# Performance work log

Hardware: AMD Instinct MI355X
Metric: run time of the kernel (lower is better)

Reference implementation:

```python
import jax, jax.numpy as jnp
import numpy as np

KNN_K = 3  # module hard-codes top-3 farthest sememes (torch.sort descending)


def setup_inputs() -> dict:
    key = jax.random.key(0)
    k1, k2, k3 = jax.random.split(key, 3)
    V, H = 50257, 1024
    L, W, S = 256, 16, 32
    embedding = jax.random.normal(k1, (V, H), dtype=jnp.float32)
    word_ids = jax.random.randint(k2, (L, W), 0, V, dtype=jnp.int32)
    sememe_ids = jax.random.randint(k3, (L, W, S), 0, V, dtype=jnp.int32)
    return {"embedding": embedding, "word_ids": word_ids, "sememe_ids": sememe_ids}


def reference(embedding, word_ids, sememe_ids):
    # embedding: [V,H]; word_ids: [L,W]; sememe_ids: [L,W,S]
    w = embedding[word_ids]                  # [L,W,H]  word embeddings (s)
    sm = embedding[sememe_ids]               # [L,W,S,H] sememe embeddings
    # F.pairwise_distance(s, sememe_tensor, p=2): L2 per sememe
    dist = jnp.linalg.norm(sm - w[:, :, None, :], axis=-1)  # [L,W,S]
    # torch.sort(distance, descending=True)[1][:3] -> 3 farthest sememes
    _, idx = jax.lax.top_k(dist, KNN_K)                      # [L,W,K]
    sel = jnp.take_along_axis(sm, idx[..., None], axis=2)    # [L,W,K,H]
    # cat([knn_mean.unsqueeze(0), s], 0).mean(0) == (knn_mean + s) / 2
    per_word = 0.5 * (sel.mean(axis=2) + w)                  # [L,W,H]
    # stack(span).mean(0): mean over words in each label
    return per_word.mean(axis=1)                             # [L,H]
```

## Files before the change

kernel.cpp:

```cpp
#include <hip/hip_runtime.h>


#define HDIM 1024
#define SNUM 32
#define WNUM 16
#define KNN  3

__global__ __launch_bounds__(256) void knn_dist_kernel(
    const float* __restrict__ emb,
    const int*   __restrict__ word_ids,
    const int*   __restrict__ sem_ids,
    float*       __restrict__ dist,
    int nj)
{
    const int wave = threadIdx.x >> 6;
    const int lane = threadIdx.x & 63;
    const int j    = blockIdx.x * 4 + wave;
    if (j >= nj) return;
    const int b    = j >> 5;

    const int wid = word_ids[b];
    const int sid = sem_ids[j];

    const float* wrow = emb + (size_t)wid * HDIM + 4 * lane;
    const float* srow = emb + (size_t)sid * HDIM + 4 * lane;

    const float4 w0 = *(const float4*)(wrow + 0);
    const float4 w1 = *(const float4*)(wrow + 256);
    const float4 w2 = *(const float4*)(wrow + 512);
    const float4 w3 = *(const float4*)(wrow + 768);
    const float4 s0 = *(const float4*)(srow + 0);
    const float4 s1 = *(const float4*)(srow + 256);
    const float4 s2 = *(const float4*)(srow + 512);
    const float4 s3 = *(const float4*)(srow + 768);

    float d = 0.0f;
    {
        float dx = s0.x - w0.x, dy = s0.y - w0.y, dz = s0.z - w0.z, dw = s0.w - w0.w;
        d += dx * dx + dy * dy + dz * dz + dw * dw;
    }
    {
        float dx = s1.x - w1.x, dy = s1.y - w1.y, dz = s1.z - w1.z, dw = s1.w - w1.w;
        d += dx * dx + dy * dy + dz * dz + dw * dw;
    }
    {
        float dx = s2.x - w2.x, dy = s2.y - w2.y, dz = s2.z - w2.z, dw = s2.w - w2.w;
        d += dx * dx + dy * dy + dz * dz + dw * dw;
    }
    {
        float dx = s3.x - w3.x, dy = s3.y - w3.y, dz = s3.z - w3.z, dw = s3.w - w3.w;
        d += dx * dx + dy * dy + dz * dz + dw * dw;
    }

    #pragma unroll
    for (int off = 32; off >= 1; off >>= 1)
        d += __shfl_xor(d, off, 64);

    if (lane == 0) dist[j] = d;
}

__global__ __launch_bounds__(256) void knn_select_kernel(
    const float* __restrict__ dist,
    const int*   __restrict__ word_ids,
    const int*   __restrict__ sem_ids,
    int*         __restrict__ sel,
    int nb)
{
    const int b = blockIdx.x * 256 + threadIdx.x;
    if (b >= nb) return;

    float dl[SNUM];
    #pragma unroll
    for (int s = 0; s < SNUM; ++s) dl[s] = dist[b * SNUM + s];

    unsigned chosen = 0;
    #pragma unroll
    for (int k = 0; k < KNN; ++k) {
        float best = -1.0f;
        int   bi   = 0;
        #pragma unroll
        for (int s = 0; s < SNUM; ++s) {
            if (!((chosen >> s) & 1u) && dl[s] > best) { best = dl[s]; bi = s; }
        }
        chosen |= (1u << bi);
        sel[b * 4 + k] = sem_ids[b * SNUM + bi];
    }
    sel[b * 4 + 3] = word_ids[b];
}

__global__ __launch_bounds__(256) void knn_out_kernel(
    const float* __restrict__ emb,
    const int*   __restrict__ sel,
    float*       __restrict__ out)
{
    const int l = blockIdx.x >> 2;
    const int q = blockIdx.x & 3;
    const int h = q * 256 + threadIdx.x;

    __shared__ int s_ids[WNUM * 4];
    if (threadIdx.x < WNUM * 4) s_ids[threadIdx.x] = sel[l * WNUM * 4 + threadIdx.x];
    __syncthreads();

    const float third = 1.0f / 3.0f;
    float acc = 0.0f;
    #pragma unroll
    for (int w = 0; w < WNUM; ++w) {
        const float e0 = emb[(size_t)s_ids[w * 4 + 0] * HDIM + h];
        const float e1 = emb[(size_t)s_ids[w * 4 + 1] * HDIM + h];
        const float e2 = emb[(size_t)s_ids[w * 4 + 2] * HDIM + h];
        const float ew = emb[(size_t)s_ids[w * 4 + 3] * HDIM + h];
        acc += (e0 + e1 + e2) * third + ew;
    }
    out[(size_t)l * HDIM + h] = acc * (0.5f / 16.0f);
}

extern "C" void kernel_launch(void* const* d_in, const int* in_sizes, int n_in,
                              void* d_out, int out_size, void* d_ws, size_t ws_size,
                              hipStream_t stream) {
    const float* emb  = (const float*)d_in[0];
    const int*   wids = (const int*)d_in[1];
    const int*   sids = (const int*)d_in[2];
    float*       out  = (float*)d_out;

    const int nb = in_sizes[1];
    const int nj = in_sizes[2];
    const int L  = out_size / HDIM;

    float* dist = (float*)d_ws;
    int*   sel  = (int*)((char*)d_ws + (size_t)nj * 4);

    knn_dist_kernel<<<dim3((nj + 3) / 4), dim3(256), 0, stream>>>(emb, wids, sids, dist, nj);
    knn_select_kernel<<<dim3((nb + 255) / 256), dim3(256), 0, stream>>>(dist, wids, sids, sel, nb);
    knn_out_kernel<<<dim3(L * 4), dim3(256), 0, stream>>>(emb, sel, out);
}
```

Baseline: 107.6 us.

## Split distance kernel by hidden-dim quarters with per-word block and partial sums

Each block now handles one word and one quarter of the hidden dimension, with each wave computing 8 sememes. The word row slice is loaded once per wave instead of once per sememe, and partial distances go to four workspace slices. The select kernel sums those four partials before doing top-3. This cuts redundant word-embedding reads and raises memory-level parallelism per wave, at the cost of a larger workspace, extra partial writes and more shuffle reductions.

```diff
diff --git a/kernel.cpp b/kernel.cpp
--- a/kernel.cpp
+++ b/kernel.cpp
@@ -10,68 +10,77 @@
     const float* __restrict__ emb,
     const int*   __restrict__ word_ids,
     const int*   __restrict__ sem_ids,
-    float*       __restrict__ dist,
+    float*       __restrict__ dist_part,
     int nj)
 {
     const int wave = threadIdx.x >> 6;
     const int lane = threadIdx.x & 63;
-    const int j    = blockIdx.x * 4 + wave;
-    if (j >= nj) return;
-    const int b    = j >> 5;
+    const int blk  = blockIdx.x;
+    const int b    = blk >> 2;
+    const int quarter = blk & 3;
 
-    const int wid = word_ids[b];
-    const int sid = sem_ids[j];
+    const int base_s = b * SNUM + wave * 8;
+    const int col    = quarter * 256 + 4 * lane;
 
-    const float* wrow = emb + (size_t)wid * HDIM + 4 * lane;
-    const float* srow = emb + (size_t)sid * HDIM + 4 * lane;
+    const int4 sa = *(const int4*)(sem_ids + base_s);
+    const int4 sb = *(const int4*)(sem_ids + base_s + 4);
+    const int  wid = word_ids[b];
 
-    const float4 w0 = *(const float4*)(wrow + 0);
-    const float4 w1 = *(const float4*)(wrow + 256);
-    const float4 w2 = *(const float4*)(wrow + 512);
-    const float4 w3 = *(const float4*)(wrow + 768);
-    const float4 s0 = *(const float4*)(srow + 0);
-    const float4 s1 = *(const float4*)(srow + 256);
-    const float4 s2 = *(const float4*)(srow + 512);
-    const float4 s3 = *(const float4*)(srow + 768);
+    const float4 w = *(const float4*)(emb + (size_t)wid * HDIM + col);
 
-    float d = 0.0f;
-    {
-        float dx = s0.x - w0.x, dy = s0.y - w0.y, dz = s0.z - w0.z, dw = s0.w - w0.w;
-        d += dx * dx + dy * dy + dz * dz + dw * dw;
-    }
-    {
-        float dx = s1.x - w1.x, dy = s1.y - w1.y, dz = s1.z - w1.z, dw = s1.w - w1.w;
-        d += dx * dx + dy * dy + dz * dz + dw * dw;
-    }
-    {
-        float dx = s2.x - w2.x, dy = s2.y - w2.y, dz = s2.z - w2.z, dw = s2.w - w2.w;
-        d += dx * dx + dy * dy + dz * dz + dw * dw;
-    }
-    {
-        float dx = s3.x - w3.x, dy = s3.y - w3.y, dz = s3.z - w3.z, dw = s3.w - w3.w;
-        d += dx * dx + dy * dy + dz * dz + dw * dw;
-    }
+    const int sids[8] = {sa.x, sa.y, sa.z, sa.w, sb.x, sb.y, sb.z, sb.w};
+    float4 sv[8];
+    #pragma unroll
+    for (int k = 0; k < 8; ++k)
+        sv[k] = *(const float4*)(emb + (size_t)sids[k] * HDIM + col);
 
     #pragma unroll
-    for (int off = 32; off >= 1; off >>= 1)
-        d += __shfl_xor(d, off, 64);
-
-    if (lane == 0) dist[j] = d;
+    for (int k = 0; k < 8; ++k) {
+        const float dx = sv[k].x - w.x;
+        const float dy = sv[k].y - w.y;
+        const float dz = sv[k].z - w.z;
+        const float dw = sv[k].w - w.w;
+        float d = (dx * dx + dy * dy) + (dz * dz + dw * dw);
+        #pragma unroll
+        for (int off = 32; off >= 1; off >>= 1)
+            d += __shfl_xor(d, off, 64);
+        if (lane == 0)
+            dist_part[(size_t)quarter * nj + base_s + k] = d;
+    }
 }
 
 __global__ __launch_bounds__(256) void knn_select_kernel(
-    const float* __restrict__ dist,
+    const float* __restrict__ dist_part,
     const int*   __restrict__ word_ids,
     const int*   __restrict__ sem_ids,
     int*         __restrict__ sel,
-    int nb)
+    int nb, int nj)
 {
     const int b = blockIdx.x * 256 + threadIdx.x;
     if (b >= nb) return;
 
+    float4 acc[8];
+    #pragma unroll
+    for (int i = 0; i < 8; ++i) acc[i] = make_float4(0.f, 0.f, 0.f, 0.f);
+
+    #pragma unroll
+    for (int q = 0; q < 4; ++q) {
+        const float4* p = (const float4*)(dist_part + (size_t)q * nj + b * SNUM);
+        #pragma unroll
+        for (int i = 0; i < 8; ++i) {
+            const float4 v = p[i];
+            acc[i].x += v.x; acc[i].y += v.y; acc[i].z += v.z; acc[i].w += v.w;
+        }
+    }
+
     float dl[SNUM];
     #pragma unroll
-    for (int s = 0; s < SNUM; ++s) dl[s] = dist[b * SNUM + s];
+    for (int i = 0; i < 8; ++i) {
+        dl[4 * i + 0] = acc[i].x;
+        dl[4 * i + 1] = acc[i].y;
+        dl[4 * i + 2] = acc[i].z;
+        dl[4 * i + 3] = acc[i].w;
+    }
 
     unsigned chosen = 0;
     #pragma unroll
@@ -126,10 +135,10 @@
     const int nj = in_sizes[2];
     const int L  = out_size / HDIM;
 
-    float* dist = (float*)d_ws;
-    int*   sel  = (int*)((char*)d_ws + (size_t)nj * 4);
+    float* dist_part = (float*)d_ws;
+    int*   sel       = (int*)((char*)d_ws + (size_t)4 * nj * 4);
 
-    knn_dist_kernel<<<dim3((nj + 3) / 4), dim3(256), 0, stream>>>(emb, wids, sids, dist, nj);
-    knn_select_kernel<<<dim3((nb + 255) / 256), dim3(256), 0, stream>>>(dist, wids, sids, sel, nb);
+    knn_dist_kernel<<<dim3(nb * 4), dim3(256), 0, stream>>>(emb, wids, sids, dist_part, nj);
+    knn_select_kernel<<<dim3((nb + 255) / 256), dim3(256), 0, stream>>>(dist_part, wids, sids, sel, nb, nj);
     knn_out_kernel<<<dim3(L * 4), dim3(256), 0, stream>>>(emb, sel, out);
 }
```

Result: faster. 91.57 us (-14.9%).

## Counting-sort sememe pairs by id before distance pass; fuse selection into output

Applied to the files above, without the earlier changes.

Adds a histogram, single-block scan and scatter that bucket the (word, sememe) pairs by sememe id, so the distance kernel visits identical embedding rows back to back for better cache reuse. The top-3 selection is folded into the output kernel, which now uses float4 loads with one block per label. This removes one launch but adds four (memset, histogram, scan, scatter), atomics, and a serial 1024-thread scan over the 50k-entry vocabulary. With random ids, few sememe ids repeat, so the reuse gain may be small next to the added overhead.

```diff
diff --git a/kernel.cpp b/kernel.cpp
--- a/kernel.cpp
+++ b/kernel.cpp
@@ -5,50 +5,100 @@
 #define SNUM 32
 #define WNUM 16
 #define KNN  3
+#define SCAN_T 1024
+#define SCAN_CHUNK 50
 
-__global__ __launch_bounds__(256) void knn_dist_kernel(
+__global__ __launch_bounds__(256) void knn_hist_kernel(
+    const int* __restrict__ sem_ids, int* __restrict__ hist, int nj)
+{
+    const int j = blockIdx.x * 256 + threadIdx.x;
+    if (j < nj) atomicAdd(&hist[sem_ids[j]], 1);
+}
+
+__global__ __launch_bounds__(SCAN_T) void knn_scan_kernel(
+    const int* __restrict__ hist, int* __restrict__ cursor, int V)
+{
+    const int t = threadIdx.x;
+    int vals[SCAN_CHUNK];
+    const int base = t * SCAN_CHUNK;
+    int sum = 0;
+    #pragma unroll
+    for (int i = 0; i < SCAN_CHUNK; ++i) {
+        const int v = base + i;
+        vals[i] = sum;
+        sum += (v < V) ? hist[v] : 0;
+    }
+    __shared__ int tot[SCAN_T];
+    tot[t] = sum;
+    __syncthreads();
+    for (int off = 1; off < SCAN_T; off <<= 1) {
+        const int x = (t >= off) ? tot[t - off] : 0;
+        __syncthreads();
+        tot[t] += x;
+        __syncthreads();
+    }
+    const int myoff = (t == 0) ? 0 : tot[t - 1];
+    #pragma unroll
+    for (int i = 0; i < SCAN_CHUNK; ++i) {
+        const int v = base + i;
+        if (v < V) cursor[v] = myoff + vals[i];
+    }
+}
+
+__global__ __launch_bounds__(256) void knn_scatter_kernel(
+    const int* __restrict__ sem_ids, int* __restrict__ cursor,
+    int* __restrict__ perm, int nj)
+{
+    const int j = blockIdx.x * 256 + threadIdx.x;
+    if (j < nj) {
+        const int pos = atomicAdd(&cursor[sem_ids[j]], 1);
+        perm[pos] = j;
+    }
+}
+
+__global__ __launch_bounds__(256) void knn_dist_sorted_kernel(
     const float* __restrict__ emb,
     const int*   __restrict__ word_ids,
     const int*   __restrict__ sem_ids,
-    float*       __restrict__ dist,
-    int nj)
+    const int*   __restrict__ perm,
+    float*       __restrict__ dist)
 {
     const int wave = threadIdx.x >> 6;
     const int lane = threadIdx.x & 63;
-    const int j    = blockIdx.x * 4 + wave;
-    if (j >= nj) return;
-    const int b    = j >> 5;
+    const int g    = blockIdx.x * 4 + wave;
 
+    const int j   = perm[g];
+    const int b   = j >> 5;
+    const int sid = sem_ids[j];
     const int wid = word_ids[b];
-    const int sid = sem_ids[j];
 
+    const float* srow = emb + (size_t)sid * HDIM + 4 * lane;
     const float* wrow = emb + (size_t)wid * HDIM + 4 * lane;
-    const float* srow = emb + (size_t)sid * HDIM + 4 * lane;
 
+    const float4 s0 = *(const float4*)(srow + 0);
+    const float4 s1 = *(const float4*)(srow + 256);
+    const float4 s2 = *(const float4*)(srow + 512);
+    const float4 s3 = *(const float4*)(srow + 768);
     const float4 w0 = *(const float4*)(wrow + 0);
     const float4 w1 = *(const float4*)(wrow + 256);
     const float4 w2 = *(const float4*)(wrow + 512);
     const float4 w3 = *(const float4*)(wrow + 768);
-    const float4 s0 = *(const float4*)(srow + 0);
-    const float4 s1 = *(const float4*)(srow + 256);
-    const float4 s2 = *(const float4*)(srow + 512);
-    const float4 s3 = *(const float4*)(srow + 768);
 
     float d = 0.0f;
     {
-        float dx = s0.x - w0.x, dy = s0.y - w0.y, dz = s0.z - w0.z, dw = s0.w - w0.w;
+        const float dx = s0.x - w0.x, dy = s0.y - w0.y, dz = s0.z - w0.z, dw = s0.w - w0.w;
         d += dx * dx + dy * dy + dz * dz + dw * dw;
     }
     {
-        float dx = s1.x - w1.x, dy = s1.y - w1.y, dz = s1.z - w1.z, dw = s1.w - w1.w;
+        const float dx = s1.x - w1.x, dy = s1.y - w1.y, dz = s1.z - w1.z, dw = s1.w - w1.w;
         d += dx * dx + dy * dy + dz * dz + dw * dw;
     }
     {
-        float dx = s2.x - w2.x, dy = s2.y - w2.y, dz = s2.z - w2.z, dw = s2.w - w2.w;
+        const float dx = s2.x - w2.x, dy = s2.y - w2.y, dz = s2.z - w2.z, dw = s2.w - w2.w;
         d += dx * dx + dy * dy + dz * dz + dw * dw;
     }
     {
-        float dx = s3.x - w3.x, dy = s3.y - w3.y, dz = s3.z - w3.z, dw = s3.w - w3.w;
+        const float dx = s3.x - w3.x, dy = s3.y - w3.y, dz = s3.z - w3.z, dw = s3.w - w3.w;
         d += dx * dx + dy * dy + dz * dz + dw * dw;
     }
 
@@ -59,59 +109,62 @@
     if (lane == 0) dist[j] = d;
 }
 
-__global__ __launch_bounds__(256) void knn_select_kernel(
+__global__ __launch_bounds__(256) void knn_outsel_kernel(
+    const float* __restrict__ emb,
     const float* __restrict__ dist,
     const int*   __restrict__ word_ids,
     const int*   __restrict__ sem_ids,
-    int*         __restrict__ sel,
-    int nb)
-{
-    const int b = blockIdx.x * 256 + threadIdx.x;
-    if (b >= nb) return;
-
-    float dl[SNUM];
-    #pragma unroll
-    for (int s = 0; s < SNUM; ++s) dl[s] = dist[b * SNUM + s];
-
-    unsigned chosen = 0;
-    #pragma unroll
-    for (int k = 0; k < KNN; ++k) {
-        float best = -1.0f;
-        int   bi   = 0;
-        #pragma unroll
-        for (int s = 0; s < SNUM; ++s) {
-            if (!((chosen >> s) & 1u) && dl[s] > best) { best = dl[s]; bi = s; }
-        }
-        chosen |= (1u << bi);
-        sel[b * 4 + k] = sem_ids[b * SNUM + bi];
-    }
-    sel[b * 4 + 3] = word_ids[b];
-}
-
-__global__ __launch_bounds__(256) void knn_out_kernel(
-    const float* __restrict__ emb,
-    const int*   __restrict__ sel,
     float*       __restrict__ out)
 {
-    const int l = blockIdx.x >> 2;
-    const int q = blockIdx.x & 3;
-    const int h = q * 256 + threadIdx.x;
+    const int l = blockIdx.x;
+    const int t = threadIdx.x;
 
     __shared__ int s_ids[WNUM * 4];
-    if (threadIdx.x < WNUM * 4) s_ids[threadIdx.x] = sel[l * WNUM * 4 + threadIdx.x];
+
+    if (t < WNUM) {
+        const int b = l * WNUM + t;
+        float dl[SNUM];
+        const float4* p = (const float4*)(dist + b * SNUM);
+        #pragma unroll
+        for (int i = 0; i < 8; ++i) {
+            const float4 v = p[i];
+            dl[4 * i + 0] = v.x;
+            dl[4 * i + 1] = v.y;
+            dl[4 * i + 2] = v.z;
+            dl[4 * i + 3] = v.w;
+        }
+        unsigned chosen = 0;
+        #pragma unroll
+        for (int k = 0; k < KNN; ++k) {
+            float best = -1.0f;
+            int   bi   = 0;
+            #pragma unroll
+            for (int s = 0; s < SNUM; ++s) {
+                if (!((chosen >> s) & 1u) && dl[s] > best) { best = dl[s]; bi = s; }
+            }
+            chosen |= (1u << bi);
+            s_ids[t * 4 + k] = sem_ids[b * SNUM + bi];
+        }
+        s_ids[t * 4 + 3] = word_ids[b];
+    }
     __syncthreads();
 
     const float third = 1.0f / 3.0f;
-    float acc = 0.0f;
-    #pragma unroll
+    float ax = 0.f, ay = 0.f, az = 0.f, aw = 0.f;
+    #pragma unroll 8
     for (int w = 0; w < WNUM; ++w) {
-        const float e0 = emb[(size_t)s_ids[w * 4 + 0] * HDIM + h];
-        const float e1 = emb[(size_t)s_ids[w * 4 + 1] * HDIM + h];
-        const float e2 = emb[(size_t)s_ids[w * 4 + 2] * HDIM + h];
-        const float ew = emb[(size_t)s_ids[w * 4 + 3] * HDIM + h];
-        acc += (e0 + e1 + e2) * third + ew;
+        const float4 e0 = *(const float4*)(emb + (size_t)s_ids[w * 4 + 0] * HDIM + 4 * t);
+        const float4 e1 = *(const float4*)(emb + (size_t)s_ids[w * 4 + 1] * HDIM + 4 * t);
+        const float4 e2 = *(const float4*)(emb + (size_t)s_ids[w * 4 + 2] * HDIM + 4 * t);
+        const float4 ew = *(const float4*)(emb + (size_t)s_ids[w * 4 + 3] * HDIM + 4 * t);
+        ax += (e0.x + e1.x + e2.x) * third + ew.x;
+        ay += (e0.y + e1.y + e2.y) * third + ew.y;
+        az += (e0.z + e1.z + e2.z) * third + ew.z;
+        aw += (e0.w + e1.w + e2.w) * third + ew.w;
     }
-    out[(size_t)l * HDIM + h] = acc * (0.5f / 16.0f);
+    const float scale = 0.5f / 16.0f;
+    *(float4*)(out + (size_t)l * HDIM + 4 * t) =
+        make_float4(ax * scale, ay * scale, az * scale, aw * scale);
 }
 
 extern "C" void kernel_launch(void* const* d_in, const int* in_sizes, int n_in,
@@ -125,11 +178,18 @@
     const int nb = in_sizes[1];
     const int nj = in_sizes[2];
     const int L  = out_size / HDIM;
+    const int V  = in_sizes[0] / HDIM;
 
-    float* dist = (float*)d_ws;
-    int*   sel  = (int*)((char*)d_ws + (size_t)nj * 4);
+    char* wsb = (char*)d_ws;
+    float* dist   = (float*)(wsb);
+    int*   perm   = (int*)(wsb + (size_t)nj * 4);
+    int*   hist   = (int*)(wsb + (size_t)nj * 8);
+    int*   cursor = (int*)(wsb + (size_t)nj * 8 + (((size_t)V * 4 + 63) & ~63ull));
 
-    knn_dist_kernel<<<dim3((nj + 3) / 4), dim3(256), 0, stream>>>(emb, wids, sids, dist, nj);
-    knn_select_kernel<<<dim3((nb + 255) / 256), dim3(256), 0, stream>>>(dist, wids, sids, sel, nb);
-    knn_out_kernel<<<dim3(L * 4), dim3(256), 0, stream>>>(emb, sel, out);
+    hipMemsetAsync(hist, 0, (size_t)V * 4, stream);
+    knn_hist_kernel<<<dim3((nj + 255) / 256), dim3(256), 0, stream>>>(sids, hist, nj);
+    knn_scan_kernel<<<dim3(1), dim3(SCAN_T), 0, stream>>>(hist, cursor, V);
+    knn_scatter_kernel<<<dim3((nj + 255) / 256), dim3(256), 0, stream>>>(sids, cursor, perm, nj);
+    knn_dist_sorted_kernel<<<dim3(nj / 4), dim3(256), 0, stream>>>(emb, wids, sids, perm, dist);
+    knn_outsel_kernel<<<dim3(L), dim3(256), 0, stream>>>(emb, dist, wids, sids, out);
 }
```

New measurement: 194.7 us. 81.0% more time.
